# Kernel tuning notes

Hardware: AMD Instinct MI355X
Metric: run time of the kernel (lower is better)

## Reference

```python
import jax, jax.numpy as jnp
import numpy as np

D_MODEL = 512
N_HEADS = 8
D_K = D_MODEL // N_HEADS
B, T = 8, 2048


def setup_inputs() -> dict:
    key = jax.random.key(0)
    ks = jax.random.split(key, 8)
    s = 0.02
    return {
        "x": jax.random.normal(ks[0], (B, T, D_MODEL), dtype=jnp.float32),
        "mask": jnp.zeros((B, T), dtype=bool),
        "ln_w": jnp.ones((D_MODEL,), dtype=jnp.float32),
        "ln_b": jnp.zeros((D_MODEL,), dtype=jnp.float32),
        "w_qkv": jax.random.normal(ks[1], (D_MODEL, 3 * D_MODEL), dtype=jnp.float32) * s,
        "b_qkv": jnp.zeros((3 * D_MODEL,), dtype=jnp.float32),
        "w_o": jax.random.normal(ks[2], (D_MODEL, D_MODEL), dtype=jnp.float32) * s,
        "b_o": jnp.zeros((D_MODEL,), dtype=jnp.float32),
    }


def _rope(q, k):
    # q, k: (B, H, T, d_k); standard GPT-NeoX-style rotary embedding
    t = q.shape[2]
    inv_freq = 1.0 / (10000.0 ** (jnp.arange(0, D_K, 2, dtype=jnp.float32) / D_K))
    ang = jnp.arange(t, dtype=jnp.float32)[:, None] * inv_freq[None, :]  # (T, d_k/2)
    cos = jnp.concatenate([jnp.cos(ang), jnp.cos(ang)], axis=-1)  # (T, d_k)
    sin = jnp.concatenate([jnp.sin(ang), jnp.sin(ang)], axis=-1)

    def rot_half(x):
        x1, x2 = x[..., : D_K // 2], x[..., D_K // 2 :]
        return jnp.concatenate([-x2, x1], axis=-1)

    q = q * cos + rot_half(q) * sin
    k = k * cos + rot_half(k) * sin
    return q, k


def reference(x, mask, ln_w, ln_b, w_qkv, b_qkv, w_o, b_o):
    Bv, Tv, Dv = x.shape
    # LayerNorm
    mu = jnp.mean(x, axis=-1, keepdims=True)
    var = jnp.mean(jnp.square(x - mu), axis=-1, keepdims=True)
    h = (x - mu) / jnp.sqrt(var + 1e-5) * ln_w + ln_b
    # QKV projection
    qkv = h @ w_qkv + b_qkv  # (B, T, 3D)
    qkv = qkv.reshape(Bv, Tv, 3, N_HEADS, D_K).transpose(2, 0, 3, 1, 4)
    q, k, v = qkv[0], qkv[1], qkv[2]  # each (B, H, T, d_k)
    q, k = _rope(q, k)
    scale = jnp.sqrt(jnp.asarray(D_K, dtype=x.dtype))
    attn = jnp.einsum("bhqd,bhkd->bhqk", q, k) / scale
    attn = jnp.where(mask[:, None, None, :], -jnp.inf, attn)
    attn = jax.nn.softmax(attn, axis=-1)
    out = jnp.einsum("bhqk,bhkd->bhqd", attn, v)  # (B, H, T, d_k)
    out = out.transpose(0, 2, 1, 3).reshape(Bv, Tv, Dv)
    return out @ w_o + b_o
```

## Files before the change

kernel.cpp:

```cpp
#include <hip/hip_runtime.h>
#include <hip/hip_bf16.h>

#define TT 2048

typedef __attribute__((ext_vector_type(8))) short bf16x8;
typedef __attribute__((ext_vector_type(4))) float f32x4;
typedef __attribute__((ext_vector_type(16))) float f32x16;
typedef __attribute__((ext_vector_type(2))) int i32x2;

__device__ __forceinline__ short f2b(float f) {
  union { float f; unsigned u; } a; a.f = f;
  unsigned r = a.u + 0x7fffu + ((a.u >> 16) & 1u);
  return (short)(r >> 16);
}
__device__ __forceinline__ unsigned cvtpk(float lo, float hi) {
  unsigned r;
  asm("v_cvt_pk_bf16_f32 %0, %1, %2" : "=v"(r) : "v"(lo), "v"(hi));
  return r;
}
__device__ __forceinline__ float max3f(float a, float b, float c) {
  float d;
  asm("v_max3_f32 %0, %1, %2, %3" : "=v"(d) : "v"(a), "v"(b), "v"(c));
  return d;
}
__device__ __forceinline__ float ex2(float x) {
#if __has_builtin(__builtin_amdgcn_exp2f)
  return __builtin_amdgcn_exp2f(x);
#else
  return exp2f(x);
#endif
}
__device__ __forceinline__ void gll16(const void* g, void* l) {
  __builtin_amdgcn_global_load_lds(
      (const __attribute__((address_space(1))) unsigned int*)g,
      (__attribute__((address_space(3))) unsigned int*)l, 16, 0, 0);
}
__device__ __forceinline__ void swap_halves(unsigned &a, unsigned &b, bool hi) {
#if __has_builtin(__builtin_amdgcn_permlane32_swap)
  i32x2 r = __builtin_amdgcn_permlane32_swap((int)a, (int)b, false, false);
  a = (unsigned)r[0]; b = (unsigned)r[1];
#else
  unsigned as = (unsigned)__shfl_xor((int)a, 32);
  unsigned bs = (unsigned)__shfl_xor((int)b, 32);
  unsigned na = hi ? bs : a;
  unsigned nb = hi ? b : as;
  a = na; b = nb;
#endif
}

__device__ __forceinline__ void p_to_frags(const f32x16 p, bool hi, bf16x8* f0, bf16x8* f1) {
  unsigned A[4][2];
#pragma unroll
  for (int u = 0; u < 4; ++u)
#pragma unroll
    for (int c = 0; c < 2; ++c)
      A[u][c] = cvtpk(p[4 * u + 2 * c], p[4 * u + 2 * c + 1]);
  swap_halves(A[0][0], A[1][0], hi);
  swap_halves(A[0][1], A[1][1], hi);
  swap_halves(A[2][0], A[3][0], hi);
  swap_halves(A[2][1], A[3][1], hi);
  union { unsigned u[4]; bf16x8 v; } r0, r1;
  r0.u[0] = A[0][0]; r0.u[1] = A[0][1]; r0.u[2] = A[1][0]; r0.u[3] = A[1][1];
  r1.u[0] = A[2][0]; r1.u[1] = A[2][1]; r1.u[2] = A[3][0]; r1.u[3] = A[3][1];
  *f0 = r0.v; *f1 = r1.v;
}

__device__ __forceinline__ bf16x8 lds16(const short* base, int row, int cb) {
  return *reinterpret_cast<const bf16x8*>(
      reinterpret_cast<const char*>(base) + row * 128 + (cb ^ ((row & 7) << 4)));
}

__global__ __launch_bounds__(256) void prep_kernel(const float* __restrict__ w_qkv,
                                                   short* __restrict__ wqkvT,
                                                   const float* __restrict__ w_o,
                                                   short* __restrict__ woT,
                                                   float2* __restrict__ tab) {
  __shared__ float t[64][65];
  const int id = blockIdx.x;
  if (id < 256) {
    const float* src; short* dst; int N, n0, k0;
    if (id < 192) { src = w_qkv; dst = wqkvT; N = 1536; n0 = (id % 24) * 64; k0 = (id / 24) * 64; }
    else { const int i2 = id - 192; src = w_o; dst = woT; N = 512; n0 = (i2 & 7) * 64; k0 = (i2 >> 3) * 64; }
    const int c = threadIdx.x & 63, r4 = threadIdx.x >> 6;
#pragma unroll
    for (int i = 0; i < 16; ++i) {
      const int r = i * 4 + r4;
      t[r][c] = src[(size_t)(k0 + r) * N + n0 + c];
    }
    __syncthreads();
#pragma unroll
    for (int i = 0; i < 16; ++i) {
      const int r = i * 4 + r4;
      dst[(size_t)(n0 + r) * 512 + k0 + c] = f2b(t[c][r]);
    }
  } else {
    const int idx = (id - 256) * 256 + threadIdx.x;
    const int i = idx & 31, tt = idx >> 5;
    const float inv_freq = __expf(-(float)i * (9.210340371976184f / 32.0f));
    float sv, cv;
    sincosf((float)tt * inv_freq, &sv, &cv);
    tab[idx] = make_float2(cv, sv);
  }
}

__global__ __launch_bounds__(256) void ln_kernel(const float* __restrict__ x,
                                                 const float* __restrict__ w,
                                                 const float* __restrict__ b,
                                                 short* __restrict__ h) {
  const int tid = threadIdx.x;
  const int row = blockIdx.x * 2 + (tid >> 7);
  const int c = tid & 127;
  const float4 v = *reinterpret_cast<const float4*>(x + (size_t)row * 512 + c * 4);
  float s = (v.x + v.y) + (v.z + v.w);
  float sq = (v.x * v.x + v.y * v.y) + (v.z * v.z + v.w * v.w);
  for (int off = 1; off < 64; off <<= 1) { s += __shfl_xor(s, off); sq += __shfl_xor(sq, off); }
  __shared__ float red[8];
  const int wv = tid >> 6;
  if ((tid & 63) == 0) { red[wv] = s; red[wv + 4] = sq; }
  __syncthreads();
  const int rb = (tid >> 7) ? 2 : 0;
  s = red[rb] + red[rb + 1];
  sq = red[rb + 4] + red[rb + 5];
  const float mu = s * (1.0f / 512.0f);
  const float var = sq * (1.0f / 512.0f) - mu * mu;
  const float inv = rsqrtf(var + 1e-5f);
  const float4 wv4 = *reinterpret_cast<const float4*>(w + c * 4);
  const float4 bv4 = *reinterpret_cast<const float4*>(b + c * 4);
  const float h0 = (v.x - mu) * inv * wv4.x + bv4.x;
  const float h1 = (v.y - mu) * inv * wv4.y + bv4.y;
  const float h2 = (v.z - mu) * inv * wv4.z + bv4.z;
  const float h3 = (v.w - mu) * inv * wv4.w + bv4.w;
  uint2 u;
  u.x = (unsigned)(unsigned short)f2b(h0) | ((unsigned)(unsigned short)f2b(h1) << 16);
  u.y = (unsigned)(unsigned short)f2b(h2) | ((unsigned)(unsigned short)f2b(h3) << 16);
  *reinterpret_cast<uint2*>(h + (size_t)row * 512 + c * 4) = u;
}

template <int EPI>
__global__ __launch_bounds__(256) void gemm128_kernel(const short* __restrict__ A,
                                                      const short* __restrict__ Bt,
                                                      const float* __restrict__ bias,
                                                      const float2* __restrict__ tab,
                                                      void* __restrict__ o0,
                                                      void* __restrict__ o1,
                                                      void* __restrict__ o2) {
  __shared__ short As[128 * 64];
  __shared__ short Bs[128 * 64];
  const int tid = threadIdx.x;
  const int lane = tid & 63, wave = tid >> 6;
  const int lr = lane & 15, lg = lane >> 4;
  const int wm = wave >> 1, wn = wave & 1;
  const int m0 = blockIdx.x * 128, n0 = blockIdx.y * 128;

  const int swz_col = ((lane & 7) ^ ((lane >> 3) & 7)) * 8;
  const short* Ag = A + (size_t)(m0 + wave * 32 + (lane >> 3)) * 512 + swz_col;
  const short* Bg = Bt + (size_t)(n0 + wave * 32 + (lane >> 3)) * 512 + swz_col;
  short* AsW = &As[(wave * 32) * 64];
  short* BsW = &Bs[(wave * 32) * 64];

  f32x4 acc[4][4] = {};

  for (int k0 = 0; k0 < 512; k0 += 64) {
#pragma unroll
    for (int i = 0; i < 4; ++i) {
      gll16(Ag + (size_t)i * 8 * 512 + k0, AsW + i * 8 * 64);
      gll16(Bg + (size_t)i * 8 * 512 + k0, BsW + i * 8 * 64);
    }
    __syncthreads();
#pragma unroll
    for (int ks = 0; ks < 2; ++ks) {
      bf16x8 af[4], bfr[4];
#pragma unroll
      for (int m = 0; m < 4; ++m)
        af[m] = lds16(As, wm * 64 + m * 16 + lr, ks * 64 + lg * 16);
#pragma unroll
      for (int n = 0; n < 4; ++n)
        bfr[n] = lds16(Bs, wn * 64 + n * 16 + lr, ks * 64 + lg * 16);
#pragma unroll
      for (int m = 0; m < 4; ++m)
#pragma unroll
        for (int n = 0; n < 4; ++n)
          acc[m][n] = __builtin_amdgcn_mfma_f32_16x16x32_bf16(af[m], bfr[n], acc[m][n], 0, 0, 0);
    }
    __syncthreads();
  }

  if (EPI == 0) {
    const int base = n0 + wn * 64;
    const int which = base >> 9;
    const int hh = (base & 511) >> 6;
    short* qp = (short*)o0; short* kp = (short*)o1; short* vtp = (short*)o2;
    const float b0 = bias[base + lr], b1 = bias[base + 16 + lr];
    const float b2 = bias[base + 32 + lr], b3 = bias[base + 48 + lr];
    const float QS = 0.125f * 1.4426950408889634f;
#pragma unroll
    for (int m = 0; m < 4; ++m) {
      const int rowb = m0 + wm * 64 + m * 16 + lg * 4;
#pragma unroll
      for (int j = 0; j < 4; ++j) {
        const int t = (rowb + j) & 2047;
        const int bh = ((rowb + j) >> 11) * 8 + hh;
        float v0 = acc[m][0][j] + b0;
        float v1 = acc[m][1][j] + b1;
        float v2 = acc[m][2][j] + b2;
        float v3 = acc[m][3][j] + b3;
        if (which < 2) {
          const float2 cs0 = tab[t * 32 + lr];
          const float2 cs1 = tab[t * 32 + 16 + lr];
          float r0 = v0 * cs0.x - v2 * cs0.y;
          float r2 = v2 * cs0.x + v0 * cs0.y;
          float r1 = v1 * cs1.x - v3 * cs1.y;
          float r3 = v3 * cs1.x + v1 * cs1.y;
          if (which == 0) { r0 *= QS; r1 *= QS; r2 *= QS; r3 *= QS; }
          short* dst = (which == 0 ? qp : kp) + ((size_t)bh * TT + t) * 64;
          dst[lr] = f2b(r0); dst[16 + lr] = f2b(r1);
          dst[32 + lr] = f2b(r2); dst[48 + lr] = f2b(r3);
        } else {
          short* vb = vtp + (size_t)bh * 64 * TT + t;
          vb[(size_t)lr * TT] = f2b(v0);
          vb[(size_t)(16 + lr) * TT] = f2b(v1);
          vb[(size_t)(32 + lr) * TT] = f2b(v2);
          vb[(size_t)(48 + lr) * TT] = f2b(v3);
        }
      }
    }
  } else {
#pragma unroll
    for (int m = 0; m < 4; ++m)
#pragma unroll
      for (int n = 0; n < 4; ++n)
#pragma unroll
        for (int j = 0; j < 4; ++j) {
          const int row = m0 + wm * 64 + m * 16 + lg * 4 + j;
          const int col = n0 + wn * 64 + n * 16 + lr;
          ((float*)o0)[(size_t)row * 512 + col] = acc[m][n][j] + bias[col];
        }
  }
}

__global__ __launch_bounds__(512) void attn_kernel(const short* __restrict__ q,
                                                   const short* __restrict__ k,
                                                   const short* __restrict__ vt,
                                                   const unsigned char* __restrict__ mask,
                                                   short* __restrict__ o) {
  __shared__ short Ks[4][64 * 64];
  __shared__ short Vs[4][64 * 64];
  __shared__ float psc[8][32];
  const int tid = threadIdx.x;
  const int lane = tid & 63, wave = tid >> 6;
  const int l31 = lane & 31, g = lane >> 5;
  const bool hi = (g != 0);
  const int nb = (blockIdx.x & 7) * 64 + (blockIdx.x >> 3);
  const int bh = nb >> 3, qt = nb & 7;
  const int bb = bh >> 3, hh = bh & 7;
  const int q0 = qt * 256 + wave * 32;
  const size_t bhT = (size_t)bh * TT;
  const unsigned char* maskb = mask + (size_t)bb * TT;

  unsigned mor = 0;
  const unsigned* mw = (const unsigned*)maskb;
#pragma unroll
  for (int i = 0; i < 8; ++i) mor |= mw[lane + 64 * i];
  const bool masked = __any((int)(mor != 0));

  bf16x8 qf[4];
#pragma unroll
  for (int ds = 0; ds < 4; ++ds)
    qf[ds] = *reinterpret_cast<const bf16x8*>(q + (bhT + q0 + l31) * 64 + ds * 16 + g * 8);

  f32x16 oa0 = {}, oa1 = {};
  float m_run = 0.0f, l_run = 0.0f;

  const int swz_col = ((lane & 7) ^ ((lane >> 3) & 7)) * 8;
  const int r0 = wave * 8;
  const short* kg0 = k + (bhT + r0 + (lane >> 3)) * 64 + swz_col;
  const short* vg0 = vt + ((size_t)bh * 64 + r0 + (lane >> 3)) * TT + swz_col;

  auto stage = [&](int kt, int buf) {
    gll16(kg0 + (size_t)kt * 4096, &Ks[buf][r0 * 64]);
    gll16(vg0 + (size_t)kt * 64,   &Vs[buf][r0 * 64]);
  };

  auto tile = [&](int kt, const short* Kc, const short* Vc) {
    f32x16 s0 = {}, s1 = {};
    __builtin_amdgcn_s_setprio(1);
#pragma unroll
    for (int ds = 0; ds < 4; ++ds) {
      const int cb = ds * 32 + g * 16;
      const bf16x8 ka0 = lds16(Kc, l31, cb);
      const bf16x8 ka1 = lds16(Kc, 32 + l31, cb);
      s0 = __builtin_amdgcn_mfma_f32_32x32x16_bf16(ka0, qf[ds], s0, 0, 0, 0);
      s1 = __builtin_amdgcn_mfma_f32_32x32x16_bf16(ka1, qf[ds], s1, 0, 0, 0);
    }
    __builtin_amdgcn_s_setprio(0);

    if (masked) {
#pragma unroll
      for (int r = 0; r < 16; ++r) {
        const int kk = (r & 3) + 8 * (r >> 2) + 4 * g;
        if (maskb[kt * 64 + kk]) s0[r] += -1e30f;
        if (maskb[kt * 64 + 32 + kk]) s1[r] += -1e30f;
      }
    }

    float b8[8];
#pragma unroll
    for (int i = 0; i < 8; ++i) b8[i] = max3f(s0[i], s0[i + 8], s1[i]);
    float c4[4];
#pragma unroll
    for (int i = 0; i < 4; ++i) c4[i] = fmaxf(s1[8 + i], s1[12 + i]);
    const float d0 = max3f(b8[0], b8[1], b8[2]);
    const float d1 = max3f(b8[3], b8[4], b8[5]);
    const float d2 = max3f(b8[6], b8[7], c4[0]);
    const float d3 = max3f(c4[1], c4[2], c4[3]);
    const float mx = fmaxf(max3f(d0, d1, d2), d3);
    const float pmax = fmaxf(mx, __shfl_xor(mx, 32));

    if (kt == 0) {
      m_run = pmax;
    } else if (!__all((int)(pmax - m_run <= 8.0f))) {
      const float nm = fmaxf(m_run, pmax);
      const float sc = ex2(m_run - nm);
      m_run = nm;
      l_run *= sc;
      if (lane < 32) psc[wave][l31] = sc;
      asm volatile("s_waitcnt lgkmcnt(0)" ::: "memory");
#pragma unroll
      for (int r = 0; r < 16; ++r) {
        const float s = psc[wave][(r & 3) + 8 * (r >> 2) + 4 * g];
        oa0[r] *= s; oa1[r] *= s;
      }
    }

#pragma unroll
    for (int i = 0; i < 16; ++i) { s0[i] = ex2(s0[i] - m_run); s1[i] = ex2(s1[i] - m_run); }

    float a8[8];
#pragma unroll
    for (int i = 0; i < 8; ++i) a8[i] = (s0[i] + s0[i + 8]) + (s1[i] + s1[i + 8]);
    const float e0 = (a8[0] + a8[1]) + (a8[2] + a8[3]);
    const float e1 = (a8[4] + a8[5]) + (a8[6] + a8[7]);
    const float rsum = e0 + e1;
    l_run += rsum + __shfl_xor(rsum, 32);

    bf16x8 pa[4];
    p_to_frags(s0, hi, &pa[0], &pa[1]);
    p_to_frags(s1, hi, &pa[2], &pa[3]);

    __builtin_amdgcn_s_setprio(1);
#pragma unroll
    for (int ks = 0; ks < 4; ++ks) {
      const int cb = ks * 32 + g * 16;
      const bf16x8 vb0 = lds16(Vc, l31, cb);
      const bf16x8 vb1 = lds16(Vc, 32 + l31, cb);
      oa0 = __builtin_amdgcn_mfma_f32_32x32x16_bf16(pa[ks], vb0, oa0, 0, 0, 0);
      oa1 = __builtin_amdgcn_mfma_f32_32x32x16_bf16(pa[ks], vb1, oa1, 0, 0, 0);
    }
    __builtin_amdgcn_s_setprio(0);
  };

  stage(0, 0);
  stage(1, 1);
  __syncthreads();

  for (int kt = 0; kt < TT / 64; kt += 2) {
    if (kt + 2 < TT / 64) stage(kt + 2, (kt + 2) & 3);
    if (kt + 3 < TT / 64) stage(kt + 3, (kt + 3) & 3);
    tile(kt,     Ks[kt & 3],       Vs[kt & 3]);
    tile(kt + 1, Ks[(kt + 1) & 3], Vs[(kt + 1) & 3]);
    __syncthreads();
  }

  const float linv = 1.0f / l_run;
#pragma unroll
  for (int r = 0; r < 16; ++r) {
    const int qr = (r & 3) + 8 * (r >> 2) + 4 * g;
    const float lv = __shfl(linv, (lane & 32) | qr, 64);
    const int trow = q0 + qr;
    const size_t orow = ((size_t)bb * TT + trow) * 512 + hh * 64 + l31;
    o[orow]      = f2b(oa0[r] * lv);
    o[orow + 32] = f2b(oa1[r] * lv);
  }
}

extern "C" void kernel_launch(void* const* d_in, const int* in_sizes, int n_in,
                              void* d_out, int out_size, void* d_ws, size_t ws_size,
                              hipStream_t stream) {
  (void)in_sizes; (void)n_in; (void)out_size; (void)ws_size;
  const float* x = (const float*)d_in[0];
  const unsigned char* mask = (const unsigned char*)d_in[1];
  const float* ln_w = (const float*)d_in[2];
  const float* ln_b = (const float*)d_in[3];
  const float* w_qkv = (const float*)d_in[4];
  const float* b_qkv = (const float*)d_in[5];
  const float* w_o = (const float*)d_in[6];
  const float* b_o = (const float*)d_in[7];
  float* out = (float*)d_out;

  char* ws = (char*)d_ws;
  short* h_buf = (short*)(ws);
  short* wqkvT = (short*)(ws + 16777216);
  short* woT   = (short*)(ws + 18350080);
  short* q_ws  = (short*)(ws + 18874368);
  short* k_ws  = (short*)(ws + 35651584);
  short* vt_ws = (short*)(ws + 52428800);
  float2* tab  = (float2*)(ws + 69206016);

  hipLaunchKernelGGL(prep_kernel, dim3(512), dim3(256), 0, stream,
                     w_qkv, wqkvT, w_o, woT, tab);
  hipLaunchKernelGGL(ln_kernel, dim3(8192), dim3(256), 0, stream, x, ln_w, ln_b, h_buf);
  hipLaunchKernelGGL((gemm128_kernel<0>), dim3(128, 12), dim3(256), 0, stream,
                     h_buf, wqkvT, b_qkv, tab, (void*)q_ws, (void*)k_ws, (void*)vt_ws);
  hipLaunchKernelGGL(attn_kernel, dim3(512), dim3(512), 0, stream,
                     q_ws, k_ws, vt_ws, mask, h_buf);
  hipLaunchKernelGGL((gemm128_kernel<1>), dim3(128, 4), dim3(256), 0, stream,
                     h_buf, woT, b_o, tab, (void*)out, nullptr, nullptr);
}
```

Baseline: 167.5 us.

## Double-buffer GEMM LDS tiles and merge layernorm into prep kernel

The GEMM main loop now uses two LDS buffers per operand. It issues the global-to-LDS loads for the next K tile before computing the current one and waits with a partial vmcnt, so memory latency overlaps with MFMA work. The layernorm kernel is folded into the weight-transpose/RoPE-table prep kernel as extra blocks, which removes one kernel launch. LDS use per GEMM block doubles, which may reduce occupancy.

```diff
diff --git a/kernel.cpp b/kernel.cpp
--- a/kernel.cpp
+++ b/kernel.cpp
@@ -70,18 +70,51 @@
       reinterpret_cast<const char*>(base) + row * 128 + (cb ^ ((row & 7) << 4)));
 }
 
-__global__ __launch_bounds__(256) void prep_kernel(const float* __restrict__ w_qkv,
-                                                   short* __restrict__ wqkvT,
-                                                   const float* __restrict__ w_o,
-                                                   short* __restrict__ woT,
-                                                   float2* __restrict__ tab) {
+__global__ __launch_bounds__(256) void prepln_kernel(const float* __restrict__ x,
+                                                     const float* __restrict__ lnw,
+                                                     const float* __restrict__ lnb,
+                                                     short* __restrict__ h,
+                                                     const float* __restrict__ w_qkv,
+                                                     short* __restrict__ wqkvT,
+                                                     const float* __restrict__ w_o,
+                                                     short* __restrict__ woT,
+                                                     float2* __restrict__ tab) {
   __shared__ float t[64][65];
   const int id = blockIdx.x;
-  if (id < 256) {
+  const int tid = threadIdx.x;
+  if (id < 8192) {
+    const int row = id * 2 + (tid >> 7);
+    const int c = tid & 127;
+    const float4 v = *reinterpret_cast<const float4*>(x + (size_t)row * 512 + c * 4);
+    float s = (v.x + v.y) + (v.z + v.w);
+    float sq = (v.x * v.x + v.y * v.y) + (v.z * v.z + v.w * v.w);
+    for (int off = 1; off < 64; off <<= 1) { s += __shfl_xor(s, off); sq += __shfl_xor(sq, off); }
+    __shared__ float red[8];
+    const int wv = tid >> 6;
+    if ((tid & 63) == 0) { red[wv] = s; red[wv + 4] = sq; }
+    __syncthreads();
+    const int rb = (tid >> 7) ? 2 : 0;
+    s = red[rb] + red[rb + 1];
+    sq = red[rb + 4] + red[rb + 5];
+    const float mu = s * (1.0f / 512.0f);
+    const float var = sq * (1.0f / 512.0f) - mu * mu;
+    const float inv = rsqrtf(var + 1e-5f);
+    const float4 wv4 = *reinterpret_cast<const float4*>(lnw + c * 4);
+    const float4 bv4 = *reinterpret_cast<const float4*>(lnb + c * 4);
+    const float h0 = (v.x - mu) * inv * wv4.x + bv4.x;
+    const float h1 = (v.y - mu) * inv * wv4.y + bv4.y;
+    const float h2 = (v.z - mu) * inv * wv4.z + bv4.z;
+    const float h3 = (v.w - mu) * inv * wv4.w + bv4.w;
+    uint2 u;
+    u.x = (unsigned)(unsigned short)f2b(h0) | ((unsigned)(unsigned short)f2b(h1) << 16);
+    u.y = (unsigned)(unsigned short)f2b(h2) | ((unsigned)(unsigned short)f2b(h3) << 16);
+    *reinterpret_cast<uint2*>(h + (size_t)row * 512 + c * 4) = u;
+  } else if (id < 8448) {
+    const int id2 = id - 8192;
     const float* src; short* dst; int N, n0, k0;
-    if (id < 192) { src = w_qkv; dst = wqkvT; N = 1536; n0 = (id % 24) * 64; k0 = (id / 24) * 64; }
-    else { const int i2 = id - 192; src = w_o; dst = woT; N = 512; n0 = (i2 & 7) * 64; k0 = (i2 >> 3) * 64; }
-    const int c = threadIdx.x & 63, r4 = threadIdx.x >> 6;
+    if (id2 < 192) { src = w_qkv; dst = wqkvT; N = 1536; n0 = (id2 % 24) * 64; k0 = (id2 / 24) * 64; }
+    else { const int i2 = id2 - 192; src = w_o; dst = woT; N = 512; n0 = (i2 & 7) * 64; k0 = (i2 >> 3) * 64; }
+    const int c = tid & 63, r4 = tid >> 6;
 #pragma unroll
     for (int i = 0; i < 16; ++i) {
       const int r = i * 4 + r4;
@@ -94,46 +127,13 @@
       dst[(size_t)(n0 + r) * 512 + k0 + c] = f2b(t[c][r]);
     }
   } else {
-    const int idx = (id - 256) * 256 + threadIdx.x;
+    const int idx = (id - 8448) * 256 + tid;
     const int i = idx & 31, tt = idx >> 5;
     const float inv_freq = __expf(-(float)i * (9.210340371976184f / 32.0f));
     float sv, cv;
     sincosf((float)tt * inv_freq, &sv, &cv);
     tab[idx] = make_float2(cv, sv);
   }
-}
-
-__global__ __launch_bounds__(256) void ln_kernel(const float* __restrict__ x,
-                                                 const float* __restrict__ w,
-                                                 const float* __restrict__ b,
-                                                 short* __restrict__ h) {
-  const int tid = threadIdx.x;
-  const int row = blockIdx.x * 2 + (tid >> 7);
-  const int c = tid & 127;
-  const float4 v = *reinterpret_cast<const float4*>(x + (size_t)row * 512 + c * 4);
-  float s = (v.x + v.y) + (v.z + v.w);
-  float sq = (v.x * v.x + v.y * v.y) + (v.z * v.z + v.w * v.w);
-  for (int off = 1; off < 64; off <<= 1) { s += __shfl_xor(s, off); sq += __shfl_xor(sq, off); }
-  __shared__ float red[8];
-  const int wv = tid >> 6;
-  if ((tid & 63) == 0) { red[wv] = s; red[wv + 4] = sq; }
-  __syncthreads();
-  const int rb = (tid >> 7) ? 2 : 0;
-  s = red[rb] + red[rb + 1];
-  sq = red[rb + 4] + red[rb + 5];
-  const float mu = s * (1.0f / 512.0f);
-  const float var = sq * (1.0f / 512.0f) - mu * mu;
-  const float inv = rsqrtf(var + 1e-5f);
-  const float4 wv4 = *reinterpret_cast<const float4*>(w + c * 4);
-  const float4 bv4 = *reinterpret_cast<const float4*>(b + c * 4);
-  const float h0 = (v.x - mu) * inv * wv4.x + bv4.x;
-  const float h1 = (v.y - mu) * inv * wv4.y + bv4.y;
-  const float h2 = (v.z - mu) * inv * wv4.z + bv4.z;
-  const float h3 = (v.w - mu) * inv * wv4.w + bv4.w;
-  uint2 u;
-  u.x = (unsigned)(unsigned short)f2b(h0) | ((unsigned)(unsigned short)f2b(h1) << 16);
-  u.y = (unsigned)(unsigned short)f2b(h2) | ((unsigned)(unsigned short)f2b(h3) << 16);
-  *reinterpret_cast<uint2*>(h + (size_t)row * 512 + c * 4) = u;
 }
 
 template <int EPI>
@@ -144,8 +144,8 @@
                                                       void* __restrict__ o0,
                                                       void* __restrict__ o1,
                                                       void* __restrict__ o2) {
-  __shared__ short As[128 * 64];
-  __shared__ short Bs[128 * 64];
+  __shared__ short As[2][128 * 64];
+  __shared__ short Bs[2][128 * 64];
   const int tid = threadIdx.x;
   const int lane = tid & 63, wave = tid >> 6;
   const int lr = lane & 15, lg = lane >> 4;
@@ -155,35 +155,47 @@
   const int swz_col = ((lane & 7) ^ ((lane >> 3) & 7)) * 8;
   const short* Ag = A + (size_t)(m0 + wave * 32 + (lane >> 3)) * 512 + swz_col;
   const short* Bg = Bt + (size_t)(n0 + wave * 32 + (lane >> 3)) * 512 + swz_col;
-  short* AsW = &As[(wave * 32) * 64];
-  short* BsW = &Bs[(wave * 32) * 64];
 
   f32x4 acc[4][4] = {};
 
-  for (int k0 = 0; k0 < 512; k0 += 64) {
+  auto stage = [&](int kk, int buf) {
 #pragma unroll
     for (int i = 0; i < 4; ++i) {
-      gll16(Ag + (size_t)i * 8 * 512 + k0, AsW + i * 8 * 64);
-      gll16(Bg + (size_t)i * 8 * 512 + k0, BsW + i * 8 * 64);
-    }
-    __syncthreads();
+      gll16(Ag + (size_t)i * 8 * 512 + kk * 64, &As[buf][(wave * 32 + i * 8) * 64]);
+      gll16(Bg + (size_t)i * 8 * 512 + kk * 64, &Bs[buf][(wave * 32 + i * 8) * 64]);
+    }
+  };
+  auto compute = [&](int buf) {
 #pragma unroll
     for (int ks = 0; ks < 2; ++ks) {
       bf16x8 af[4], bfr[4];
 #pragma unroll
       for (int m = 0; m < 4; ++m)
-        af[m] = lds16(As, wm * 64 + m * 16 + lr, ks * 64 + lg * 16);
+        af[m] = lds16(As[buf], wm * 64 + m * 16 + lr, ks * 64 + lg * 16);
 #pragma unroll
       for (int n = 0; n < 4; ++n)
-        bfr[n] = lds16(Bs, wn * 64 + n * 16 + lr, ks * 64 + lg * 16);
+        bfr[n] = lds16(Bs[buf], wn * 64 + n * 16 + lr, ks * 64 + lg * 16);
 #pragma unroll
       for (int m = 0; m < 4; ++m)
 #pragma unroll
         for (int n = 0; n < 4; ++n)
           acc[m][n] = __builtin_amdgcn_mfma_f32_16x16x32_bf16(af[m], bfr[n], acc[m][n], 0, 0, 0);
     }
-    __syncthreads();
+  };
+
+  stage(0, 0);
+  for (int kk = 0; kk < 7; ++kk) {
+    stage(kk + 1, (kk + 1) & 1);
+    asm volatile("s_waitcnt vmcnt(8)" ::: "memory");
+    __builtin_amdgcn_s_barrier();
+    __builtin_amdgcn_sched_barrier(0);
+    compute(kk & 1);
+    __builtin_amdgcn_s_barrier();
   }
+  asm volatile("s_waitcnt vmcnt(0)" ::: "memory");
+  __builtin_amdgcn_s_barrier();
+  __builtin_amdgcn_sched_barrier(0);
+  compute(1);
 
   if (EPI == 0) {
     const int base = n0 + wn * 64;
@@ -406,9 +418,8 @@
   short* vt_ws = (short*)(ws + 52428800);
   float2* tab  = (float2*)(ws + 69206016);
 
-  hipLaunchKernelGGL(prep_kernel, dim3(512), dim3(256), 0, stream,
-                     w_qkv, wqkvT, w_o, woT, tab);
-  hipLaunchKernelGGL(ln_kernel, dim3(8192), dim3(256), 0, stream, x, ln_w, ln_b, h_buf);
+  hipLaunchKernelGGL(prepln_kernel, dim3(8704), dim3(256), 0, stream,
+                     x, ln_w, ln_b, h_buf, w_qkv, wqkvT, w_o, woT, tab);
   hipLaunchKernelGGL((gemm128_kernel<0>), dim3(128, 12), dim3(256), 0, stream,
                      h_buf, wqkvT, b_qkv, tab, (void*)q_ws, (void*)k_ws, (void*)vt_ws);
   hipLaunchKernelGGL(attn_kernel, dim3(512), dim3(512), 0, stream,
```

Measured after the change: 164.5 us. About the same (-1.8%).
